# Optimization experiments

Measured on AMD Instinct MI355X. Metric: run time of the kernel, lower is better.

Reference implementation:

```python
import jax, jax.numpy as jnp
import numpy as np


def setup_inputs() -> dict:
    key = jax.random.key(0)
    x = jax.random.normal(key, (16, 3, 512, 512), dtype=jnp.float32)
    return {"x": x}


def reference(x):
    # x: [B, C, H, W] with H, W even.
    B, C, H, W = x.shape
    # --- single-level 2D Haar DWT (pywt 'haar' convention) ---
    # View each 2x2 block: a=top-left, b=top-right, c=bottom-left, d=bottom-right.
    blocks = x.reshape(B, C, H // 2, 2, W // 2, 2)
    a = blocks[:, :, :, 0, :, 0]
    b = blocks[:, :, :, 0, :, 1]
    c = blocks[:, :, :, 1, :, 0]
    d = blocks[:, :, :, 1, :, 1]
    half = jnp.asarray(0.5, x.dtype)
    LL = (a + b + c + d) * half  # cA
    LH = (a + b - c - d) * half  # cH (horizontal detail)
    HL = (a - b + c - d) * half  # cV (vertical detail)
    HH = (a - b - c + d) * half  # cD (diagonal detail)
    # [B, C, 4, H/2, W/2]
    sub = jnp.stack([LL, LH, HL, HH], axis=2)
    # Bilinear upsample back to (H, W); jax.image bilinear uses half-pixel
    # centers, matching F.interpolate(mode='bilinear', align_corners=False).
    up = jax.image.resize(sub, (B, C, 4, H, W), method="bilinear")
    # IG: original channel resized to its own size -> identity under this mode.
    bands = jnp.concatenate([x[:, :, None], up], axis=2)  # [B, C, 5, H, W]
    return bands.reshape(B, 5 * C, H, W)
```

## Files before the change

### kernel.cpp

```cpp
#include <hip/hip_runtime.h>

#define BC   48
#define HF   512
#define WF   512
#define HH   256
#define WH   256
#define TK   4
#define TL   128
#define HW   (HF * WF)

typedef float v4 __attribute__((ext_vector_type(4)));
typedef float v2 __attribute__((ext_vector_type(2)));

__global__ __launch_bounds__(256) void wavelet_kernel(const float* __restrict__ x,
                                                      float* __restrict__ out) {
    __shared__ v4 coef[2][TK + 2][TL / 2 + 1];

    const int tx = threadIdx.x;
    const int ty = threadIdx.y;
    const int k0 = blockIdx.y * TK;
    const int l0 = blockIdx.x * TL;
    const int bc = blockIdx.z;

    const float* __restrict__ xin = x + (size_t)bc * HW;

    const int t = ty * 64 + tx;
    for (int i = t; i < (TK + 2) * (TL + 2); i += 256) {
        const int ry = i / (TL + 2);
        const int rx = i - ry * (TL + 2);
        int k = k0 + ry - 1; k = k < 0 ? 0 : (k > HH - 1 ? HH - 1 : k);
        int l = l0 + rx - 1; l = l < 0 ? 0 : (l > WH - 1 ? WH - 1 : l);
        const float* p = xin + (size_t)(2 * k) * WF + 2 * l;
        const v2 top = *reinterpret_cast<const v2*>(p);
        const v2 bot = *reinterpret_cast<const v2*>(p + WF);
        const float a = top.x, b = top.y, c = bot.x, d = bot.y;
        v4 v;
        v.x = (a + b + c + d) * 0.5f;
        v.y = (a + b - c - d) * 0.5f;
        v.z = (a - b + c - d) * 0.5f;
        v.w = (a - b - c + d) * 0.5f;
        coef[rx & 1][ry][rx >> 1] = v;
    }
    __syncthreads();

    v4 hr[3][4];
#pragma unroll
    for (int r = 0; r < 3; ++r) {
        const v4 A = coef[0][ty + r][tx];
        const v4 B = coef[1][ty + r][tx];
        const v4 C = coef[0][ty + r][tx + 1];
        const v4 D = coef[1][ty + r][tx + 1];
        hr[r][0] = A * 0.25f + B * 0.75f;
        hr[r][1] = B * 0.75f + C * 0.25f;
        hr[r][2] = B * 0.25f + C * 0.75f;
        hr[r][3] = C * 0.75f + D * 0.25f;
    }
    v4 ve[4], vo[4];
#pragma unroll
    for (int j = 0; j < 4; ++j) {
        ve[j] = hr[0][j] * 0.25f + hr[1][j] * 0.75f;
        vo[j] = hr[1][j] * 0.75f + hr[2][j] * 0.25f;
    }

    const int y0 = 2 * (k0 + ty);
    const int x0 = 2 * l0 + 4 * tx;
    float* __restrict__ outp = out + (size_t)bc * 5 * HW;

    {
        const v4 t0 = *reinterpret_cast<const v4*>(xin + (size_t)y0 * WF + x0);
        const v4 t1 = *reinterpret_cast<const v4*>(xin + (size_t)(y0 + 1) * WF + x0);
        __builtin_nontemporal_store(t0, reinterpret_cast<v4*>(outp + (size_t)y0 * WF + x0));
        __builtin_nontemporal_store(t1, reinterpret_cast<v4*>(outp + (size_t)(y0 + 1) * WF + x0));
    }
#define STORE_BAND(BIDX, COMP)                                                         \
    {                                                                                  \
        v4 e, o;                                                                       \
        e.x = ve[0].COMP; e.y = ve[1].COMP; e.z = ve[2].COMP; e.w = ve[3].COMP;        \
        o.x = vo[0].COMP; o.y = vo[1].COMP; o.z = vo[2].COMP; o.w = vo[3].COMP;        \
        float* ob = outp + (size_t)BIDX * HW;                                          \
        __builtin_nontemporal_store(e, reinterpret_cast<v4*>(ob + (size_t)y0 * WF + x0)); \
        __builtin_nontemporal_store(o, reinterpret_cast<v4*>(ob + (size_t)(y0 + 1) * WF + x0)); \
    }
    STORE_BAND(1, x)
    STORE_BAND(2, y)
    STORE_BAND(3, z)
    STORE_BAND(4, w)
#undef STORE_BAND
}

extern "C" void kernel_launch(void* const* d_in, const int* in_sizes, int n_in,
                              void* d_out, int out_size, void* d_ws, size_t ws_size,
                              hipStream_t stream) {
    const float* x = (const float*)d_in[0];
    float* out = (float*)d_out;
    dim3 grid(WH / TL, HH / TK, BC);
    dim3 block(64, 4);
    hipLaunchKernelGGL(wavelet_kernel, grid, block, 0, stream, x, out);
}
```

Measured before the change: 280.9 us.

## Drop shared-memory tile and compute Haar halo directly from global loads per thread

```diff
diff --git a/kernel.cpp b/kernel.cpp
--- a/kernel.cpp
+++ b/kernel.cpp
@@ -1,85 +1,113 @@
 #include <hip/hip_runtime.h>
 
-#define BC   48
 #define HF   512
 #define WF   512
 #define HH   256
-#define WH   256
+#define HW   (HF * WF)
 #define TK   4
-#define TL   128
-#define HW   (HF * WF)
 
 typedef float v4 __attribute__((ext_vector_type(4)));
 typedef float v2 __attribute__((ext_vector_type(2)));
 
-__global__ __launch_bounds__(256) void wavelet_kernel(const float* __restrict__ x,
-                                                      float* __restrict__ out) {
-    __shared__ v4 coef[2][TK + 2][TL / 2 + 1];
+__device__ __forceinline__ v4 haar2(float a, float b, float c, float d) {
+    const float s1 = a + b, d1 = a - b, s2 = c + d, d2 = c - d;
+    v4 v;
+    v.x = (s1 + s2) * 0.5f;
+    v.y = (s1 - s2) * 0.5f;
+    v.z = (d1 + d2) * 0.5f;
+    v.w = (d1 - d2) * 0.5f;
+    return v;
+}
 
+__global__ __launch_bounds__(256, 2) void wavelet_kernel(const float* __restrict__ x,
+                                                         float* __restrict__ out) {
     const int tx = threadIdx.x;
     const int ty = threadIdx.y;
-    const int k0 = blockIdx.y * TK;
-    const int l0 = blockIdx.x * TL;
+    const int k  = blockIdx.y * TK + ty;
+    const int l0 = blockIdx.x * 128;
     const int bc = blockIdx.z;
 
-    const float* __restrict__ xin = x + (size_t)bc * HW;
+    const float* __restrict__ xin  = x   + (size_t)bc * HW;
+    float*       __restrict__ outp = out + (size_t)bc * (size_t)(5 * HW);
 
-    const int t = ty * 64 + tx;
-    for (int i = t; i < (TK + 2) * (TL + 2); i += 256) {
-        const int ry = i / (TL + 2);
-        const int rx = i - ry * (TL + 2);
-        int k = k0 + ry - 1; k = k < 0 ? 0 : (k > HH - 1 ? HH - 1 : k);
-        int l = l0 + rx - 1; l = l < 0 ? 0 : (l > WH - 1 ? WH - 1 : l);
-        const float* p = xin + (size_t)(2 * k) * WF + 2 * l;
-        const v2 top = *reinterpret_cast<const v2*>(p);
-        const v2 bot = *reinterpret_cast<const v2*>(p + WF);
-        const float a = top.x, b = top.y, c = bot.x, d = bot.y;
-        v4 v;
-        v.x = (a + b + c + d) * 0.5f;
-        v.y = (a + b - c - d) * 0.5f;
-        v.z = (a - b + c - d) * 0.5f;
-        v.w = (a - b - c + d) * 0.5f;
-        coef[rx & 1][ry][rx >> 1] = v;
+    const int x0 = 2 * l0 + 4 * tx;
+    const int xl = (x0 == 0) ? 0 : x0 - 2;
+    const int xr = (x0 + 4 > WF - 2) ? WF - 2 : x0 + 4;
+
+    const int ku = (k == 0) ? 0 : k - 1;
+    const int kd = (k == HH - 1) ? HH - 1 : k + 1;
+
+    const float* p0 = xin + (size_t)(2 * ku) * WF;
+    const float* p1 = xin + (size_t)(2 * k)  * WF;
+    const float* p2 = xin + (size_t)(2 * kd) * WF;
+
+    const v4 t0  = *reinterpret_cast<const v4*>(p0 + x0);
+    const v4 u0  = *reinterpret_cast<const v4*>(p0 + WF + x0);
+    const v2 tl0 = *reinterpret_cast<const v2*>(p0 + xl);
+    const v2 ul0 = *reinterpret_cast<const v2*>(p0 + WF + xl);
+    const v2 tr0 = *reinterpret_cast<const v2*>(p0 + xr);
+    const v2 ur0 = *reinterpret_cast<const v2*>(p0 + WF + xr);
+
+    const v4 t1  = *reinterpret_cast<const v4*>(p1 + x0);
+    const v4 u1  = *reinterpret_cast<const v4*>(p1 + WF + x0);
+    const v2 tl1 = *reinterpret_cast<const v2*>(p1 + xl);
+    const v2 ul1 = *reinterpret_cast<const v2*>(p1 + WF + xl);
+    const v2 tr1 = *reinterpret_cast<const v2*>(p1 + xr);
+    const v2 ur1 = *reinterpret_cast<const v2*>(p1 + WF + xr);
+
+    const v4 t2  = *reinterpret_cast<const v4*>(p2 + x0);
+    const v4 u2  = *reinterpret_cast<const v4*>(p2 + WF + x0);
+    const v2 tl2 = *reinterpret_cast<const v2*>(p2 + xl);
+    const v2 ul2 = *reinterpret_cast<const v2*>(p2 + WF + xl);
+    const v2 tr2 = *reinterpret_cast<const v2*>(p2 + xr);
+    const v2 ur2 = *reinterpret_cast<const v2*>(p2 + WF + xr);
+
+    v4 ve[4], vo[4];
+    {
+        const v4 A = haar2(tl0.x, tl0.y, ul0.x, ul0.y);
+        const v4 B = haar2(t0.x,  t0.y,  u0.x,  u0.y);
+        const v4 C = haar2(t0.z,  t0.w,  u0.z,  u0.w);
+        const v4 D = haar2(tr0.x, tr0.y, ur0.x, ur0.y);
+        ve[0] = (A * 0.25f + B * 0.75f) * 0.25f;
+        ve[1] = (B * 0.75f + C * 0.25f) * 0.25f;
+        ve[2] = (B * 0.25f + C * 0.75f) * 0.25f;
+        ve[3] = (C * 0.75f + D * 0.25f) * 0.25f;
     }
-    __syncthreads();
-
-    v4 hr[3][4];
-#pragma unroll
-    for (int r = 0; r < 3; ++r) {
-        const v4 A = coef[0][ty + r][tx];
-        const v4 B = coef[1][ty + r][tx];
-        const v4 C = coef[0][ty + r][tx + 1];
-        const v4 D = coef[1][ty + r][tx + 1];
-        hr[r][0] = A * 0.25f + B * 0.75f;
-        hr[r][1] = B * 0.75f + C * 0.25f;
-        hr[r][2] = B * 0.25f + C * 0.75f;
-        hr[r][3] = C * 0.75f + D * 0.25f;
+    {
+        const v4 A = haar2(tl1.x, tl1.y, ul1.x, ul1.y);
+        const v4 B = haar2(t1.x,  t1.y,  u1.x,  u1.y);
+        const v4 C = haar2(t1.z,  t1.w,  u1.z,  u1.w);
+        const v4 D = haar2(tr1.x, tr1.y, ur1.x, ur1.y);
+        v4 h;
+        h = A * 0.25f + B * 0.75f;  ve[0] += h * 0.75f;  vo[0] = h * 0.75f;
+        h = B * 0.75f + C * 0.25f;  ve[1] += h * 0.75f;  vo[1] = h * 0.75f;
+        h = B * 0.25f + C * 0.75f;  ve[2] += h * 0.75f;  vo[2] = h * 0.75f;
+        h = C * 0.75f + D * 0.25f;  ve[3] += h * 0.75f;  vo[3] = h * 0.75f;
     }
-    v4 ve[4], vo[4];
-#pragma unroll
-    for (int j = 0; j < 4; ++j) {
-        ve[j] = hr[0][j] * 0.25f + hr[1][j] * 0.75f;
-        vo[j] = hr[1][j] * 0.75f + hr[2][j] * 0.25f;
+    {
+        const v4 A = haar2(tl2.x, tl2.y, ul2.x, ul2.y);
+        const v4 B = haar2(t2.x,  t2.y,  u2.x,  u2.y);
+        const v4 C = haar2(t2.z,  t2.w,  u2.z,  u2.w);
+        const v4 D = haar2(tr2.x, tr2.y, ur2.x, ur2.y);
+        vo[0] += (A * 0.25f + B * 0.75f) * 0.25f;
+        vo[1] += (B * 0.75f + C * 0.25f) * 0.25f;
+        vo[2] += (B * 0.25f + C * 0.75f) * 0.25f;
+        vo[3] += (C * 0.75f + D * 0.25f) * 0.25f;
     }
 
-    const int y0 = 2 * (k0 + ty);
-    const int x0 = 2 * l0 + 4 * tx;
-    float* __restrict__ outp = out + (size_t)bc * 5 * HW;
+    const int y0 = 2 * k;
+    float* o0 = outp + (size_t)y0 * WF + x0;
+    __builtin_nontemporal_store(t1, reinterpret_cast<v4*>(o0));
+    __builtin_nontemporal_store(u1, reinterpret_cast<v4*>(o0 + WF));
 
-    {
-        const v4 t0 = *reinterpret_cast<const v4*>(xin + (size_t)y0 * WF + x0);
-        const v4 t1 = *reinterpret_cast<const v4*>(xin + (size_t)(y0 + 1) * WF + x0);
-        __builtin_nontemporal_store(t0, reinterpret_cast<v4*>(outp + (size_t)y0 * WF + x0));
-        __builtin_nontemporal_store(t1, reinterpret_cast<v4*>(outp + (size_t)(y0 + 1) * WF + x0));
-    }
 #define STORE_BAND(BIDX, COMP)                                                         \
     {                                                                                  \
         v4 e, o;                                                                       \
         e.x = ve[0].COMP; e.y = ve[1].COMP; e.z = ve[2].COMP; e.w = ve[3].COMP;        \
         o.x = vo[0].COMP; o.y = vo[1].COMP; o.z = vo[2].COMP; o.w = vo[3].COMP;        \
-        float* ob = outp + (size_t)BIDX * HW;                                          \
-        __builtin_nontemporal_store(e, reinterpret_cast<v4*>(ob + (size_t)y0 * WF + x0)); \
-        __builtin_nontemporal_store(o, reinterpret_cast<v4*>(ob + (size_t)(y0 + 1) * WF + x0)); \
+        float* ob = outp + (size_t)BIDX * HW + (size_t)y0 * WF + x0;                   \
+        __builtin_nontemporal_store(e, reinterpret_cast<v4*>(ob));                     \
+        __builtin_nontemporal_store(o, reinterpret_cast<v4*>(ob + WF));                \
     }
     STORE_BAND(1, x)
     STORE_BAND(2, y)
@@ -93,7 +121,7 @@
                               hipStream_t stream) {
     const float* x = (const float*)d_in[0];
     float* out = (float*)d_out;
-    dim3 grid(WH / TL, HH / TK, BC);
-    dim3 block(64, 4);
+    dim3 grid(2, HH / TK, 48);
+    dim3 block(64, TK);
     hipLaunchKernelGGL(wavelet_kernel, grid, block, 0, stream, x, out);
 }
```

After: 282.0 us. No clear change (+0.4%).
